# Kernel optimization log

Hardware: AMD Instinct MI355X
Metric: run time of the kernel (lower is better)

Reference implementation:

```python
import jax, jax.numpy as jnp
import numpy as np

N, M = 2048, 2048
NODE_DIM = 64
HIDDEN_DIM = 64  # must equal NODE_DIM due to broadcast in msg = weights * h_r
LN_EPS = 1e-5


def setup_inputs() -> dict:
    key = jax.random.key(0)
    ks = jax.random.split(key, 14)
    s_edge1 = 1.0 / np.sqrt(4.0)
    s_edge2 = 1.0 / np.sqrt(HIDDEN_DIM)
    s_n1 = 1.0 / np.sqrt(NODE_DIM + HIDDEN_DIM)
    s_n2 = 1.0 / np.sqrt(NODE_DIM)
    return {
        "h_l": jax.random.normal(ks[0], (N, NODE_DIM), jnp.float32),
        "x_l": jax.random.normal(ks[1], (N, 3), jnp.float32),
        "h_r": jax.random.normal(ks[2], (M, NODE_DIM), jnp.float32),
        "x_r": jax.random.normal(ks[3], (M, 3), jnp.float32),
        # edge_mlp: Linear(4, hidden), SiLU, Linear(hidden, hidden)
        "W1": jax.random.uniform(ks[4], (4, HIDDEN_DIM), jnp.float32, -s_edge1, s_edge1),
        "b1": jax.random.uniform(ks[5], (HIDDEN_DIM,), jnp.float32, -s_edge1, s_edge1),
        "W2": jax.random.uniform(ks[6], (HIDDEN_DIM, HIDDEN_DIM), jnp.float32, -s_edge2, s_edge2),
        "b2": jax.random.uniform(ks[7], (HIDDEN_DIM,), jnp.float32, -s_edge2, s_edge2),
        # node_update: Linear(node+hidden, node), LayerNorm(node), SiLU, Linear(node, node)
        "Wn1": jax.random.uniform(ks[8], (NODE_DIM + HIDDEN_DIM, NODE_DIM), jnp.float32, -s_n1, s_n1),
        "bn1": jax.random.uniform(ks[9], (NODE_DIM,), jnp.float32, -s_n1, s_n1),
        "ln_g": jnp.ones((NODE_DIM,), jnp.float32),
        "ln_b": jnp.zeros((NODE_DIM,), jnp.float32),
        "Wn2": jax.random.uniform(ks[10], (NODE_DIM, NODE_DIM), jnp.float32, -s_n2, s_n2),
        "bn2": jax.random.uniform(ks[11], (NODE_DIM,), jnp.float32, -s_n2, s_n2),
    }


def _forward(h_l, x_l, h_r, x_r, W1, b1, W2, b2, Wn1, bn1, ln_g, ln_b, Wn2, bn2):
    # squared pairwise distances [N, M]
    d2 = jnp.sum((x_l[:, None, :] - x_r[None, :, :]) ** 2, axis=-1)
    dist_feat = jnp.exp(-d2 / 5.0)
    # chemical-property interaction matrices from last 3 node features
    l_p, r_p = h_l[:, -3:], h_r[:, -3:]
    hbond = l_p[:, 0:1] * r_p[:, 1:2].T + l_p[:, 1:2] * r_p[:, 0:1].T  # [N, M]
    hydro = l_p[:, 2:3] * r_p[:, 2:3].T                                # [N, M]
    edge_raw = jnp.stack([dist_feat, hbond, hydro, jnp.ones_like(d2)], axis=-1)  # [N, M, 4]
    # edge MLP -> sigmoid gating weights [N, M, H]
    e = jax.nn.silu(edge_raw @ W1 + b1) @ W2 + b2
    w = jax.nn.sigmoid(e)
    # weighted, normalized aggregation over M
    h_agg = jnp.einsum('nmh,mh->nh', w, h_r) / (jnp.sum(w, axis=1) + 1e-6)
    # node update MLP with LayerNorm
    z = jnp.concatenate([h_l, h_agg], axis=-1) @ Wn1 + bn1
    mu = jnp.mean(z, axis=-1, keepdims=True)
    var = jnp.var(z, axis=-1, keepdims=True)
    z = (z - mu) / jnp.sqrt(var + LN_EPS) * ln_g + ln_b
    z = jax.nn.silu(z) @ Wn2 + bn2
    return h_l + z


def reference(h_l, x_l, h_r, x_r, W1, b1, W2, b2, Wn1, bn1, ln_g, ln_b, Wn2, bn2):
    return _forward(h_l, x_l, h_r, x_r, W1, b1, W2, b2, Wn1, bn1, ln_g, ln_b, Wn2, bn2)
```

## Files before the change

kernel.cpp:

```cpp
#include <hip/hip_runtime.h>
#include <hip/hip_bf16.h>


#define NTOT 2048
#define MTOT 2048
#define MSPLIT 32
#define MCHUNK 64

typedef short bf16x8 __attribute__((ext_vector_type(8)));
typedef float f32x4  __attribute__((ext_vector_type(4)));
typedef float f32x2  __attribute__((ext_vector_type(2)));
typedef int   i32x4  __attribute__((ext_vector_type(4)));

#define NL2E (-1.4426950408889634f)
#define C1E  (-0.2885390081777927f)

__device__ __forceinline__ float fast_exp2(float x) {
#if __has_builtin(__builtin_amdgcn_exp2f)
  return __builtin_amdgcn_exp2f(x);
#else
  return __exp2f(x);
#endif
}
__device__ __forceinline__ float fast_rcp(float x) {
#if __has_builtin(__builtin_amdgcn_rcpf)
  return __builtin_amdgcn_rcpf(x);
#else
  return 1.0f / x;
#endif
}
__device__ __forceinline__ float fast_rsq(float x) {
#if __has_builtin(__builtin_amdgcn_rsqf)
  return __builtin_amdgcn_rsqf(x);
#else
  return rsqrtf(x);
#endif
}
__device__ __forceinline__ f32x2 pk_fma(f32x2 a, f32x2 b, f32x2 c) {
  return __builtin_elementwise_fma(a, b, c);
}

__device__ __forceinline__ short to_bf16_rne(float x) {
  union { float f; unsigned u; } v; v.f = x;
  unsigned r = v.u + 0x7FFFu + ((v.u >> 16) & 1u);
  return (short)(r >> 16);
}

__device__ __forceinline__ unsigned pack_bf16_rn(float lo, float hi) {
  union { float f; unsigned u; } a, b;
  a.f = lo; b.f = hi;
  unsigned au = a.u + 0x8000u, bu = b.u + 0x8000u;
#if __has_builtin(__builtin_amdgcn_perm)
  return __builtin_amdgcn_perm(bu, au, 0x07060302u);
#else
  return (au >> 16) | (bu & 0xffff0000u);
#endif
}

__global__ __launch_bounds__(256, 2)
void edge_kernel(const float* __restrict__ h_l,
                 const float* __restrict__ x_l,
                 const float* __restrict__ h_r,
                 const float* __restrict__ x_r,
                 const float* __restrict__ W1,
                 const float* __restrict__ b1,
                 const float* __restrict__ W2,
                 const float* __restrict__ b2,
                 float* __restrict__ num_g,
                 float* __restrict__ den_g) {
  __shared__ float hr_s[MCHUNK][64];
  __shared__ float xr_s[MCHUNK][8];

  const int tid  = threadIdx.x;
  const int wave = tid >> 6;
  const int lane = tid & 63;
  const int l15  = lane & 15;
  const int quad = lane >> 4;

  const int nblk   = blockIdx.x / MSPLIT;
  const int msplit = blockIdx.x % MSPLIT;
  const int n0     = nblk * 64 + wave * 16;
  const int mBase  = msplit * MCHUNK;

  const int nA = n0 + l15;
  const float xl0 = x_l[nA * 3 + 0];
  const float xl1 = x_l[nA * 3 + 1];
  const float xl2 = x_l[nA * 3 + 2];
  const float lp0 = h_l[nA * 64 + 61];
  const float lp1 = h_l[nA * 64 + 62];
  const float lp2 = h_l[nA * 64 + 63];

  f32x2 w1d2[8], w1h2[8], w1y2[8], b1p2[8];
#pragma unroll
  for (int p = 0; p < 8; ++p) {
    const int j0 = 2 * p, j1 = 2 * p + 1;
    const int hA = (j0 < 8) ? (quad * 8 + j0) : (32 + quad * 8 + (j0 - 8));
    const int hB = (j1 < 8) ? (quad * 8 + j1) : (32 + quad * 8 + (j1 - 8));
    w1d2[p] = f32x2{W1[0 * 64 + hA], W1[0 * 64 + hB]};
    w1h2[p] = f32x2{W1[1 * 64 + hA], W1[1 * 64 + hB]};
    w1y2[p] = f32x2{W1[2 * 64 + hA], W1[2 * 64 + hB]};
    b1p2[p] = f32x2{b1[hA] + W1[3 * 64 + hA], b1[hB] + W1[3 * 64 + hB]};
  }

  bf16x8 Bfrag[4][2];
#pragma unroll
  for (int c = 0; c < 4; ++c) {
#pragma unroll
    for (int h = 0; h < 2; ++h) {
      bf16x8 f;
#pragma unroll
      for (int j = 0; j < 8; ++j) {
        const int k = h * 32 + quad * 8 + j;
        f[j] = to_bf16_rne(W2[k * 64 + c * 16 + l15]);
      }
      Bfrag[c][h] = f;
    }
  }

  f32x2 b2c2[4];
#pragma unroll
  for (int c = 0; c < 4; ++c) {
    const float v = NL2E * b2[c * 16 + l15];
    b2c2[c] = f32x2{v, v};
  }

  for (int idx = tid; idx < MCHUNK * 64; idx += 256) {
    const int mm = idx >> 6, hh = idx & 63;
    hr_s[mm][hh] = h_r[(mBase + mm) * 64 + hh];
  }
  for (int idx = tid; idx < MCHUNK * 8; idx += 256) {
    const int mm = idx >> 3, k = idx & 7;
    float v = 0.f;
    const int m = mBase + mm;
    if (k < 3)      v = x_r[m * 3 + k];
    else if (k < 6) v = h_r[m * 64 + 61 + (k - 3)];
    xr_s[mm][k] = v;
  }

  const f32x4 zero4 = {0.f, 0.f, 0.f, 0.f};
  const f32x2 one2 = {1.f, 1.f};
  const f32x2 nl2e2 = {NL2E, NL2E};
  f32x2 numr2[4][2], denr2[4][2];
#pragma unroll
  for (int c = 0; c < 4; ++c)
#pragma unroll
    for (int h = 0; h < 2; ++h) {
      numr2[c][h] = f32x2{0.f, 0.f};
      denr2[c][h] = f32x2{0.f, 0.f};
    }

  __syncthreads();

#pragma unroll 2
  for (int ms = 0; ms < MCHUNK; ++ms) {
    const float xr0 = xr_s[ms][0], xr1 = xr_s[ms][1], xr2 = xr_s[ms][2];
    const float rp0 = xr_s[ms][3], rp1 = xr_s[ms][4], rp2 = xr_s[ms][5];
    const float dx = xl0 - xr0, dy = xl1 - xr1, dz = xl2 - xr2;
    const float d2 = fmaf(dz, dz, fmaf(dy, dy, dx * dx));
    const float dist = fast_exp2(d2 * C1E);
    const float hb = fmaf(lp1, rp0, lp0 * rp1);
    const float hy = lp2 * rp2;
    const f32x2 distv = {dist, dist};
    const f32x2 hbv = {hb, hb};
    const f32x2 hyv = {hy, hy};

    f32x2 s2[8];
#pragma unroll
    for (int p = 0; p < 8; ++p) {
      const f32x2 t2 = pk_fma(distv, w1d2[p],
                       pk_fma(hbv, w1h2[p],
                       pk_fma(hyv, w1y2[p], b1p2[p])));
      const f32x2 a2 = t2 * nl2e2;
      f32x2 e2;
      e2.x = fast_exp2(a2.x);
      e2.y = fast_exp2(a2.y);
      const f32x2 dden = e2 + one2;
      f32x2 r2;
      r2.x = fast_rcp(dden.x);
      r2.y = fast_rcp(dden.y);
      s2[p] = t2 * r2;
    }
    i32x4 p0, p1;
    p0.x = pack_bf16_rn(s2[0].x, s2[0].y);  p0.y = pack_bf16_rn(s2[1].x, s2[1].y);
    p0.z = pack_bf16_rn(s2[2].x, s2[2].y);  p0.w = pack_bf16_rn(s2[3].x, s2[3].y);
    p1.x = pack_bf16_rn(s2[4].x, s2[4].y);  p1.y = pack_bf16_rn(s2[5].x, s2[5].y);
    p1.z = pack_bf16_rn(s2[6].x, s2[6].y);  p1.w = pack_bf16_rn(s2[7].x, s2[7].y);
    const bf16x8 A0 = __builtin_bit_cast(bf16x8, p0);
    const bf16x8 A1 = __builtin_bit_cast(bf16x8, p1);

    f32x4 acc[4];
#pragma unroll
    for (int c = 0; c < 4; ++c) {
      acc[c] = __builtin_amdgcn_mfma_f32_16x16x32_bf16(A0, Bfrag[c][0], zero4, 0, 0, 0);
      acc[c] = __builtin_amdgcn_mfma_f32_16x16x32_bf16(A1, Bfrag[c][1], acc[c], 0, 0, 0);
    }

#pragma unroll
    for (int c = 0; c < 4; ++c) {
      const float hrv = hr_s[ms][c * 16 + l15];
      const f32x2 hrv2 = {hrv, hrv};
#pragma unroll
      for (int h = 0; h < 2; ++h) {
        const f32x2 a2 = {acc[c][2 * h], acc[c][2 * h + 1]};
        const f32x2 arg = pk_fma(a2, nl2e2, b2c2[c]);
        f32x2 e2;
        e2.x = fast_exp2(arg.x);
        e2.y = fast_exp2(arg.y);
        const f32x2 dden = e2 + one2;
        f32x2 w2;
        w2.x = fast_rcp(dden.x);
        w2.y = fast_rcp(dden.y);
        numr2[c][h] = pk_fma(w2, hrv2, numr2[c][h]);
        denr2[c][h] = denr2[c][h] + w2;
      }
    }
  }

#pragma unroll
  for (int c = 0; c < 4; ++c)
#pragma unroll
    for (int h = 0; h < 2; ++h)
#pragma unroll
      for (int k = 0; k < 2; ++k) {
        const int r = 2 * h + k;
        const int n = n0 + quad * 4 + r;
        const int h2 = c * 16 + l15;
        atomicAdd(&num_g[n * 64 + h2], k ? numr2[c][h].y : numr2[c][h].x);
        atomicAdd(&den_g[n * 64 + h2], k ? denr2[c][h].y : denr2[c][h].x);
      }
}

__global__ __launch_bounds__(256)
void node_kernel(const float* __restrict__ h_l,
                 const float* __restrict__ num_g,
                 const float* __restrict__ den_g,
                 const float* __restrict__ Wn1,
                 const float* __restrict__ bn1,
                 const float* __restrict__ ln_g,
                 const float* __restrict__ ln_b,
                 const float* __restrict__ Wn2,
                 const float* __restrict__ bn2,
                 float* __restrict__ out) {
  __shared__ float Wn1_s[128 * 64];
  __shared__ float Wn2_s[64 * 64];
  __shared__ float xbuf[4][128];
  __shared__ float zbuf[4][64];

  const int tid = threadIdx.x;
  for (int i = tid; i < 128 * 64; i += 256) Wn1_s[i] = Wn1[i];
  for (int i = tid; i < 64 * 64; i += 256) Wn2_s[i] = Wn2[i];

  const int wave = tid >> 6, lane = tid & 63;
  const int row = blockIdx.x * 4 + wave;

  const float hl = h_l[row * 64 + lane];
  const float dn = den_g[row * 64 + lane] + 1e-6f;
  const float hagg = num_g[row * 64 + lane] * fast_rcp(dn);
  xbuf[wave][lane] = hl;
  xbuf[wave][64 + lane] = hagg;
  __syncthreads();

  float t = bn1[lane];
#pragma unroll 8
  for (int k = 0; k < 128; ++k) t = fmaf(xbuf[wave][k], Wn1_s[k * 64 + lane], t);

  float s1 = t, s2 = t * t;
#pragma unroll
  for (int off = 32; off; off >>= 1) {
    s1 += __shfl_xor(s1, off);
    s2 += __shfl_xor(s2, off);
  }
  const float mu = s1 * 0.015625f;
  const float var = fmaf(s2, 0.015625f, -mu * mu);
  const float rs = fast_rsq(var + 1e-5f);
  const float zn = fmaf((t - mu) * rs, ln_g[lane], ln_b[lane]);
  const float sz = zn * fast_rcp(1.0f + fast_exp2(zn * NL2E));
  zbuf[wave][lane] = sz;
  __syncthreads();

  float o = bn2[lane];
#pragma unroll 8
  for (int k = 0; k < 64; ++k) o = fmaf(zbuf[wave][k], Wn2_s[k * 64 + lane], o);

  out[row * 64 + lane] = hl + o;
}

extern "C" void kernel_launch(void* const* d_in, const int* in_sizes, int n_in,
                              void* d_out, int out_size, void* d_ws, size_t ws_size,
                              hipStream_t stream) {
  const float* h_l = (const float*)d_in[0];
  const float* x_l = (const float*)d_in[1];
  const float* h_r = (const float*)d_in[2];
  const float* x_r = (const float*)d_in[3];
  const float* W1  = (const float*)d_in[4];
  const float* b1  = (const float*)d_in[5];
  const float* W2  = (const float*)d_in[6];
  const float* b2  = (const float*)d_in[7];
  const float* Wn1 = (const float*)d_in[8];
  const float* bn1 = (const float*)d_in[9];
  const float* lng = (const float*)d_in[10];
  const float* lnb = (const float*)d_in[11];
  const float* Wn2 = (const float*)d_in[12];
  const float* bn2 = (const float*)d_in[13];

  float* num_g = (float*)d_ws;
  float* den_g = num_g + (size_t)NTOT * 64;

  hipMemsetAsync(d_ws, 0, (size_t)NTOT * 64 * 2 * sizeof(float), stream);
  edge_kernel<<<dim3((NTOT / 64) * MSPLIT), dim3(256), 0, stream>>>(
      h_l, x_l, h_r, x_r, W1, b1, W2, b2, num_g, den_g);
  node_kernel<<<dim3(NTOT / 4), dim3(256), 0, stream>>>(
      h_l, num_g, den_g, Wn1, bn1, lng, lnb, Wn2, bn2, (float*)d_out);
}
```

Baseline: 223.6 us.

## Compute edge-MLP first layer in packed fp16 and use f16 MFMA

Moves the first edge-MLP layer, including the SiLU, from packed fp32 to packed half2 arithmetic with half exp2 and rcp. The hidden activations now feed the MFMA directly as fp16, which drops the manual bf16 packing, and W2 is converted to fp16 instead of bf16. The h_r tile in shared memory is transposed so each lane fetches its four hr values with one vector load, and the x_r row is read with vector loads. The aim is to halve the transcendental and FMA work in the hot inner loop. The cost is reduced precision, with fp16 range limits on the SiLU intermediates.

```diff
diff --git a/kernel.cpp b/kernel.cpp
--- a/kernel.cpp
+++ b/kernel.cpp
@@ -1,5 +1,6 @@
 #include <hip/hip_runtime.h>
 #include <hip/hip_bf16.h>
+#include <hip/hip_fp16.h>
 
 
 #define NTOT 2048
@@ -7,7 +8,7 @@
 #define MSPLIT 32
 #define MCHUNK 64
 
-typedef short bf16x8 __attribute__((ext_vector_type(8)));
+typedef _Float16 f16x8 __attribute__((ext_vector_type(8)));
 typedef float f32x4  __attribute__((ext_vector_type(4)));
 typedef float f32x2  __attribute__((ext_vector_type(2)));
 typedef int   i32x4  __attribute__((ext_vector_type(4)));
@@ -38,23 +39,6 @@
 }
 __device__ __forceinline__ f32x2 pk_fma(f32x2 a, f32x2 b, f32x2 c) {
   return __builtin_elementwise_fma(a, b, c);
-}
-
-__device__ __forceinline__ short to_bf16_rne(float x) {
-  union { float f; unsigned u; } v; v.f = x;
-  unsigned r = v.u + 0x7FFFu + ((v.u >> 16) & 1u);
-  return (short)(r >> 16);
-}
-
-__device__ __forceinline__ unsigned pack_bf16_rn(float lo, float hi) {
-  union { float f; unsigned u; } a, b;
-  a.f = lo; b.f = hi;
-  unsigned au = a.u + 0x8000u, bu = b.u + 0x8000u;
-#if __has_builtin(__builtin_amdgcn_perm)
-  return __builtin_amdgcn_perm(bu, au, 0x07060302u);
-#else
-  return (au >> 16) | (bu & 0xffff0000u);
-#endif
 }
 
 __global__ __launch_bounds__(256, 2)
@@ -68,7 +52,7 @@
                  const float* __restrict__ b2,
                  float* __restrict__ num_g,
                  float* __restrict__ den_g) {
-  __shared__ float hr_s[MCHUNK][64];
+  __shared__ float hrT[MCHUNK][64];
   __shared__ float xr_s[MCHUNK][8];
 
   const int tid  = threadIdx.x;
@@ -90,28 +74,29 @@
   const float lp1 = h_l[nA * 64 + 62];
   const float lp2 = h_l[nA * 64 + 63];
 
-  f32x2 w1d2[8], w1h2[8], w1y2[8], b1p2[8];
+  __half2 w1d2[8], w1h2[8], w1y2[8], b1p2[8];
 #pragma unroll
   for (int p = 0; p < 8; ++p) {
     const int j0 = 2 * p, j1 = 2 * p + 1;
     const int hA = (j0 < 8) ? (quad * 8 + j0) : (32 + quad * 8 + (j0 - 8));
     const int hB = (j1 < 8) ? (quad * 8 + j1) : (32 + quad * 8 + (j1 - 8));
-    w1d2[p] = f32x2{W1[0 * 64 + hA], W1[0 * 64 + hB]};
-    w1h2[p] = f32x2{W1[1 * 64 + hA], W1[1 * 64 + hB]};
-    w1y2[p] = f32x2{W1[2 * 64 + hA], W1[2 * 64 + hB]};
-    b1p2[p] = f32x2{b1[hA] + W1[3 * 64 + hA], b1[hB] + W1[3 * 64 + hB]};
-  }
-
-  bf16x8 Bfrag[4][2];
+    w1d2[p] = __floats2half2_rn(W1[0 * 64 + hA], W1[0 * 64 + hB]);
+    w1h2[p] = __floats2half2_rn(W1[1 * 64 + hA], W1[1 * 64 + hB]);
+    w1y2[p] = __floats2half2_rn(W1[2 * 64 + hA], W1[2 * 64 + hB]);
+    b1p2[p] = __floats2half2_rn(b1[hA] + W1[3 * 64 + hA],
+                                b1[hB] + W1[3 * 64 + hB]);
+  }
+
+  f16x8 Bfrag[4][2];
 #pragma unroll
   for (int c = 0; c < 4; ++c) {
 #pragma unroll
     for (int h = 0; h < 2; ++h) {
-      bf16x8 f;
+      f16x8 f;
 #pragma unroll
       for (int j = 0; j < 8; ++j) {
         const int k = h * 32 + quad * 8 + j;
-        f[j] = to_bf16_rne(W2[k * 64 + c * 16 + l15]);
+        f[j] = (_Float16)W2[k * 64 + c * 16 + l15];
       }
       Bfrag[c][h] = f;
     }
@@ -125,8 +110,9 @@
   }
 
   for (int idx = tid; idx < MCHUNK * 64; idx += 256) {
-    const int mm = idx >> 6, hh = idx & 63;
-    hr_s[mm][hh] = h_r[(mBase + mm) * 64 + hh];
+    const int mm = idx >> 6, w = idx & 63;
+    const int i = w >> 2, c = w & 3;
+    hrT[mm][w] = h_r[(mBase + mm) * 64 + c * 16 + i];
   }
   for (int idx = tid; idx < MCHUNK * 8; idx += 256) {
     const int mm = idx >> 3, k = idx & 7;
@@ -140,6 +126,8 @@
   const f32x4 zero4 = {0.f, 0.f, 0.f, 0.f};
   const f32x2 one2 = {1.f, 1.f};
   const f32x2 nl2e2 = {NL2E, NL2E};
+  const __half2 nl2eh = __float2half2_rn(NL2E);
+  const __half2 oneh  = __float2half2_rn(1.0f);
   f32x2 numr2[4][2], denr2[4][2];
 #pragma unroll
   for (int c = 0; c < 4; ++c)
@@ -153,52 +141,48 @@
 
 #pragma unroll 2
   for (int ms = 0; ms < MCHUNK; ++ms) {
-    const float xr0 = xr_s[ms][0], xr1 = xr_s[ms][1], xr2 = xr_s[ms][2];
-    const float rp0 = xr_s[ms][3], rp1 = xr_s[ms][4], rp2 = xr_s[ms][5];
-    const float dx = xl0 - xr0, dy = xl1 - xr1, dz = xl2 - xr2;
+    const f32x4 xa = *(const f32x4*)&xr_s[ms][0];
+    const f32x2 xb = *(const f32x2*)&xr_s[ms][4];
+    const float dx = xl0 - xa[0], dy = xl1 - xa[1], dz = xl2 - xa[2];
     const float d2 = fmaf(dz, dz, fmaf(dy, dy, dx * dx));
     const float dist = fast_exp2(d2 * C1E);
-    const float hb = fmaf(lp1, rp0, lp0 * rp1);
-    const float hy = lp2 * rp2;
-    const f32x2 distv = {dist, dist};
-    const f32x2 hbv = {hb, hb};
-    const f32x2 hyv = {hy, hy};
-
-    f32x2 s2[8];
+    const float hb = fmaf(lp1, xa[3], lp0 * xb[0]);
+    const float hy = lp2 * xb[1];
+    const __half2 dist2 = __float2half2_rn(dist);
+    const __half2 hb2 = __float2half2_rn(hb);
+    const __half2 hy2 = __float2half2_rn(hy);
+
+    __half2 s2[8];
 #pragma unroll
     for (int p = 0; p < 8; ++p) {
-      const f32x2 t2 = pk_fma(distv, w1d2[p],
-                       pk_fma(hbv, w1h2[p],
-                       pk_fma(hyv, w1y2[p], b1p2[p])));
-      const f32x2 a2 = t2 * nl2e2;
-      f32x2 e2;
-      e2.x = fast_exp2(a2.x);
-      e2.y = fast_exp2(a2.y);
-      const f32x2 dden = e2 + one2;
-      f32x2 r2;
-      r2.x = fast_rcp(dden.x);
-      r2.y = fast_rcp(dden.y);
-      s2[p] = t2 * r2;
+      const __half2 t2 = __hfma2(dist2, w1d2[p],
+                         __hfma2(hb2, w1h2[p],
+                         __hfma2(hy2, w1y2[p], b1p2[p])));
+      const __half2 a2 = __hmul2(t2, nl2eh);
+      const __half2 e2 = h2exp2(a2);
+      const __half2 dden = __hadd2(e2, oneh);
+      const __half2 r2 = h2rcp(dden);
+      s2[p] = __hmul2(t2, r2);
     }
     i32x4 p0, p1;
-    p0.x = pack_bf16_rn(s2[0].x, s2[0].y);  p0.y = pack_bf16_rn(s2[1].x, s2[1].y);
-    p0.z = pack_bf16_rn(s2[2].x, s2[2].y);  p0.w = pack_bf16_rn(s2[3].x, s2[3].y);
-    p1.x = pack_bf16_rn(s2[4].x, s2[4].y);  p1.y = pack_bf16_rn(s2[5].x, s2[5].y);
-    p1.z = pack_bf16_rn(s2[6].x, s2[6].y);  p1.w = pack_bf16_rn(s2[7].x, s2[7].y);
-    const bf16x8 A0 = __builtin_bit_cast(bf16x8, p0);
-    const bf16x8 A1 = __builtin_bit_cast(bf16x8, p1);
+    p0.x = __builtin_bit_cast(int, s2[0]);  p0.y = __builtin_bit_cast(int, s2[1]);
+    p0.z = __builtin_bit_cast(int, s2[2]);  p0.w = __builtin_bit_cast(int, s2[3]);
+    p1.x = __builtin_bit_cast(int, s2[4]);  p1.y = __builtin_bit_cast(int, s2[5]);
+    p1.z = __builtin_bit_cast(int, s2[6]);  p1.w = __builtin_bit_cast(int, s2[7]);
+    const f16x8 A0 = __builtin_bit_cast(f16x8, p0);
+    const f16x8 A1 = __builtin_bit_cast(f16x8, p1);
 
     f32x4 acc[4];
 #pragma unroll
     for (int c = 0; c < 4; ++c) {
-      acc[c] = __builtin_amdgcn_mfma_f32_16x16x32_bf16(A0, Bfrag[c][0], zero4, 0, 0, 0);
-      acc[c] = __builtin_amdgcn_mfma_f32_16x16x32_bf16(A1, Bfrag[c][1], acc[c], 0, 0, 0);
-    }
-
+      acc[c] = __builtin_amdgcn_mfma_f32_16x16x32_f16(A0, Bfrag[c][0], zero4, 0, 0, 0);
+      acc[c] = __builtin_amdgcn_mfma_f32_16x16x32_f16(A1, Bfrag[c][1], acc[c], 0, 0, 0);
+    }
+
+    const f32x4 hrv4 = *(const f32x4*)&hrT[ms][l15 * 4];
 #pragma unroll
     for (int c = 0; c < 4; ++c) {
-      const float hrv = hr_s[ms][c * 16 + l15];
-      const f32x2 hrv2 = {hrv, hrv};
+      const f32x2 hrv2 = {hrv4[c], hrv4[c]};
 #pragma unroll
       for (int h = 0; h < 2; ++h) {
         const f32x2 a2 = {acc[c][2 * h], acc[c][2 * h + 1]};
```

Result: faster. 217.4 us (-2.8%).
